# Kernel optimization log

Hardware: AMD Instinct MI355X
Metric: run time of the kernel (lower is better)

Reference implementation:

```python
import jax, jax.numpy as jnp
import numpy as np

B = 4096      # batch
D_IN = 512    # input_dim
D = 256       # d_model
T = 424       # n_targets
L = 6         # num_layers
EPS = 1e-5    # torch LayerNorm default


def _ln(x, g, b):
    m = jnp.mean(x, axis=-1, keepdims=True)
    v = jnp.var(x, axis=-1, keepdims=True)
    return (x - m) * jax.lax.rsqrt(v + EPS) * g + b


def setup_inputs() -> dict:
    key = jax.random.key(0)
    ks = iter(jax.random.split(key, 32))
    r = lambda shape, s=0.05: jax.random.normal(next(ks), shape, dtype=jnp.float32) * s
    return {
        'x': jax.random.normal(next(ks), (B, D_IN), dtype=jnp.float32),
        'proj_W': r((4, D // 4, D_IN)), 'proj_b': r((4, D // 4)),
        'attn_in_W': r((L, 3 * D, D)), 'attn_in_b': r((L, 3 * D)),
        'attn_out_W': r((L, D, D)), 'attn_out_b': r((L, D)),
        'ln_g': jnp.ones((L, D), jnp.float32), 'ln_b': jnp.zeros((L, D), jnp.float32),
        'ff_W1': r((L, 4 * D, D)), 'ff_b1': r((L, 4 * D)),
        'ff_W2': r((L, D, 4 * D)), 'ff_b2': r((L, D)),
        'cross_in_W': r((3 * D, D)), 'cross_in_b': r((3 * D,)),
        'cross_out_W': r((D, D)), 'cross_out_b': r((D,)),
        'tp_W1': r((T, D // 2, D)), 'tp_b1': r((T, D // 2)),
        'tp_ln_g': jnp.ones((T, D // 2), jnp.float32), 'tp_ln_b': jnp.zeros((T, D // 2), jnp.float32),
        'tp_W2': r((T, D // 4, D // 2)), 'tp_b2': r((T, D // 4)),
        'tp_W3': r((T, D // 4)), 'tp_b3': r((T,)),
    }


def reference(x, proj_W, proj_b, attn_in_W, attn_in_b, attn_out_W, attn_out_b,
              ln_g, ln_b, ff_W1, ff_b1, ff_W2, ff_b2,
              cross_in_W, cross_in_b, cross_out_W, cross_out_b,
              tp_W1, tp_b1, tp_ln_g, tp_ln_b, tp_W2, tp_b2, tp_W3, tp_b3):
    # 4 feature projections -> concat == reshape of stacked einsum  [B, 4, D/4] -> [B, D]
    h = jnp.einsum('bd,pkd->bpk', x, proj_W) + proj_b
    h = h.reshape(h.shape[0], D)

    # 6 transformer blocks on seq_len=1: softmax over a single key == 1, so
    # MHA(x,x,x) reduces exactly to out_proj(v_proj(x)); dropout = identity (eval).
    for i in range(L):
        Wv, bv = attn_in_W[i, 2 * D:], attn_in_b[i, 2 * D:]
        attn = (h @ Wv.T + bv) @ attn_out_W[i].T + attn_out_b[i]
        h = _ln(h + attn, ln_g[i], ln_b[i])          # same norm instance reused
        ff = jax.nn.gelu(h @ ff_W1[i].T + ff_b1[i], approximate=False) @ ff_W2[i].T + ff_b2[i]
        h = _ln(h + ff, ln_g[i], ln_b[i])

    # cross-target attention, also seq_len=1 -> v/out projections only
    Wv, bv = cross_in_W[2 * D:], cross_in_b[2 * D:]
    h = h + ((h @ Wv.T + bv) @ cross_out_W.T + cross_out_b)

    # 424 per-target MLP heads, batched as grouped GEMMs
    t = jnp.einsum('bd,tkd->btk', h, tp_W1) + tp_b1          # [B, T, 128]
    t = jax.nn.relu(_ln(t, tp_ln_g, tp_ln_b))
    t = jax.nn.relu(jnp.einsum('btk,tmk->btm', t, tp_W2) + tp_b2)  # [B, T, 64]
    out = jnp.einsum('btm,tm->bt', t, tp_W3) + tp_b3         # [B, T]
    return out
```

## Files before the change

### kernel.cpp

```cpp
#include <hip/hip_runtime.h>
#include <stdint.h>
#include <utility>
#include <type_traits>

using bf16x8 = __attribute__((ext_vector_type(8))) short;
using f32x4  = __attribute__((ext_vector_type(4))) float;

__device__ __forceinline__ f32x4 mfma16(bf16x8 a, bf16x8 b, f32x4 c) {
  return __builtin_amdgcn_mfma_f32_16x16x32_bf16(a, b, c, 0, 0, 0);
}

__device__ __forceinline__ unsigned short f2b_rne(float f) {
  union { float f; unsigned u; } v; v.f = f;
  unsigned r = v.u + 0x7fffu + ((v.u >> 16) & 1u);
  return (unsigned short)(r >> 16);
}

__device__ __forceinline__ void gload16(const void* g, void* l) {
  __builtin_amdgcn_global_load_lds(
      (const __attribute__((address_space(1))) void*)g,
      (__attribute__((address_space(3))) void*)l, 16, 0, 0);
}

template<int N> __device__ __forceinline__ void vmwait() {
  if constexpr (N <= 0)      asm volatile("s_waitcnt vmcnt(0)" ::: "memory");
  else if constexpr (N == 1) asm volatile("s_waitcnt vmcnt(1)" ::: "memory");
  else if constexpr (N == 2) asm volatile("s_waitcnt vmcnt(2)" ::: "memory");
  else if constexpr (N == 3) asm volatile("s_waitcnt vmcnt(3)" ::: "memory");
  else if constexpr (N == 4) asm volatile("s_waitcnt vmcnt(4)" ::: "memory");
  else                       asm volatile("s_waitcnt vmcnt(5)" ::: "memory");
}

template<class F, int... Is>
__device__ __forceinline__ void sfor_impl(F&& f, std::integer_sequence<int, Is...>) {
  (f(std::integral_constant<int, Is>{}), ...);
}
template<int N, class F>
__device__ __forceinline__ void sfor(F&& f) {
  sfor_impl(static_cast<F&&>(f), std::make_integer_sequence<int, N>{});
}

__device__ __forceinline__ void stage1(const unsigned short* __restrict__ W, int K,
                                       int col0, int kt, char* slot, int lane) {
  const int ci = lane >> 2, kc = lane & 3;
  const unsigned short* src = W + (size_t)(col0 + ci) * K + kt * 32
                              + (((kc * 16) ^ ((ci & 3) << 4)) >> 1);
  gload16(src, slot);
}

template<int NCG, int AS, int K>
__device__ __forceinline__ void gemm_pipe3(const unsigned short* __restrict__ W, int c0,
                                           const char* __restrict__ abuf,
                                           char* __restrict__ ring, int lane,
                                           f32x4 (&acc)[NCG]) {
  const int r = lane & 15, hi16 = (lane >> 4) << 4;
  const int swz7 = (r & 7) << 4, swz3 = (r & 3) << 4;
  constexpr int NKT = K / 32;
  constexpr int TILES = NCG * NKT;
  constexpr int DEPTH = (TILES < 5) ? TILES : 5;
  sfor<DEPTH>([&](auto pc) {
    constexpr int p = pc.value;
    stage1(W, K, c0 + (p % NCG) * 16, p / NCG, ring + (p % 6) * 1024, lane);
  });
  bf16x8 areg;
  sfor<TILES>([&](auto tc) {
    constexpr int t = tc.value;
    constexpr int kt = t / NCG, cg = t % NCG;
    constexpr int REM = TILES - 1 - t;
    vmwait<(REM < 4 ? REM : 4)>();
    __builtin_amdgcn_sched_barrier(0);
    if constexpr (t + 5 < TILES) {
      constexpr int t5 = t + 5;
      stage1(W, K, c0 + (t5 % NCG) * 16, t5 / NCG, ring + (t5 % 6) * 1024, lane);
    }
    if constexpr (cg == 0)
      areg = *reinterpret_cast<const bf16x8*>(abuf + r * AS + ((kt * 64 + hi16) ^ swz7));
    const bf16x8 b = *reinterpret_cast<const bf16x8*>(
        ring + (t % 6) * 1024 + r * 64 + (hi16 ^ swz3));
    acc[cg] = mfma16(areg, b, acc[cg]);
  });
}

__global__ void f2b_kernel(const float* __restrict__ s, unsigned short* __restrict__ d, int n4) {
  int i = blockIdx.x * 256 + threadIdx.x;
  if (i >= n4) return;
  float4 v = reinterpret_cast<const float4*>(s)[i];
  ushort4 o;
  o.x = f2b_rne(v.x); o.y = f2b_rne(v.y); o.z = f2b_rne(v.z); o.w = f2b_rne(v.w);
  reinterpret_cast<ushort4*>(d)[i] = o;
}

__global__ __launch_bounds__(256) void compose_attn(
    const float* __restrict__ aiW, const float* __restrict__ aib,
    const float* __restrict__ aoW, const float* __restrict__ aob,
    const float* __restrict__ ciW, const float* __restrict__ cib,
    const float* __restrict__ coW, const float* __restrict__ cob,
    unsigned short* __restrict__ wEff, float* __restrict__ bEff) {
  const int mat = blockIdx.y;
  const float* Wo = (mat < 6) ? aoW + (size_t)mat * 65536 : coW;
  const float* Wv = (mat < 6) ? aiW + (size_t)mat * 196608 + 131072 : ciW + 131072;
  const float* bv = (mat < 6) ? aib + mat * 768 + 512 : cib + 512;
  const float* bo = (mat < 6) ? aob + mat * 256 : cob;
  unsigned short* Wd = wEff + (size_t)mat * 65536;
  const int m = blockIdx.x * 16 + (threadIdx.x >> 4);
  const int k0 = (threadIdx.x & 15) * 16;
  float c[16] = {};
  for (int j = 0; j < 256; ++j) {
    const float a = Wo[m * 256 + j];
    const float* Br = Wv + j * 256 + k0;
#pragma unroll
    for (int kk = 0; kk < 16; ++kk) c[kk] = fmaf(a, Br[kk], c[kk]);
  }
#pragma unroll
  for (int kk = 0; kk < 16; ++kk) Wd[m * 256 + k0 + kk] = f2b_rne(c[kk]);
  if (blockIdx.x == 0) {
    const int mm = threadIdx.x;
    float s = 0.f;
    for (int j = 0; j < 256; ++j) s = fmaf(Wo[mm * 256 + j], bv[j], s);
    bEff[mat * 256 + mm] = s + bo[mm];
  }
}

__global__ __launch_bounds__(1024) void trunk_fused(
    const unsigned short* __restrict__ xb, const unsigned short* __restrict__ pWb,
    const float* __restrict__ projb,
    const unsigned short* __restrict__ wEff, const float* __restrict__ bEff,
    const unsigned short* __restrict__ f1Wb, const float* __restrict__ f1b,
    const unsigned short* __restrict__ f2Wb, const float* __restrict__ f2bp,
    const float* __restrict__ lng, const float* __restrict__ lnb,
    unsigned short* __restrict__ hbf) {
  __shared__ char hbuf[16 * 512];
  __shared__ char gbuf[16 * 2048];
  __shared__ char ringbuf[16 * 6144];
  __shared__ float red[2][16][16];
  const int tid = threadIdx.x, wid = tid >> 6, lane = tid & 63;
  const int r = lane & 15, hi = lane >> 4;
  const int row0 = blockIdx.x << 4;
  const int col = wid * 16 + r;
  char* ring = ringbuf + wid * 6144;

  {
    const int row = tid >> 6, c8 = tid & 63;
    bf16x8 v = *reinterpret_cast<const bf16x8*>(xb + (size_t)(row0 + row) * 512 + c8 * 8);
    *reinterpret_cast<bf16x8*>(gbuf + row * 1024 + ((c8 * 16) ^ ((row & 7) << 4))) = v;
  }
  __syncthreads();

  f32x4 hreg;

  auto store_hb = [&]() {
    const int cb = col * 2;
#pragma unroll
    for (int j = 0; j < 4; ++j) {
      const int row = hi * 4 + j;
      *reinterpret_cast<unsigned short*>(hbuf + row * 512 + (cb ^ ((row & 7) << 4))) =
          f2b_rne(hreg[j]);
    }
  };

  auto ln_apply = [&](float gm, float bb) {
    float sum[4], sq[4];
#pragma unroll
    for (int j = 0; j < 4; ++j) { sum[j] = hreg[j]; sq[j] = hreg[j] * hreg[j]; }
#pragma unroll
    for (int m = 1; m < 16; m <<= 1)
#pragma unroll
      for (int j = 0; j < 4; ++j) {
        sum[j] += __shfl_xor(sum[j], m, 64);
        sq[j]  += __shfl_xor(sq[j],  m, 64);
      }
    if (r == 0)
#pragma unroll
      for (int j = 0; j < 4; ++j) {
        red[0][hi * 4 + j][wid] = sum[j];
        red[1][hi * 4 + j][wid] = sq[j];
      }
    __syncthreads();
#pragma unroll
    for (int j = 0; j < 4; ++j) {
      const int row = hi * 4 + j;
      float ts = 0.f, tq = 0.f;
#pragma unroll
      for (int q = 0; q < 4; ++q) {
        f32x4 p = *reinterpret_cast<const f32x4*>(&red[0][row][q * 4]);
        f32x4 s2 = *reinterpret_cast<const f32x4*>(&red[1][row][q * 4]);
        ts += p[0] + p[1] + p[2] + p[3];
        tq += s2[0] + s2[1] + s2[2] + s2[3];
      }
      const float mean = ts * (1.f / 256.f);
      const float rstd = rsqrtf(tq * (1.f / 256.f) - mean * mean + 1e-5f);
      hreg[j] = (hreg[j] - mean) * rstd * gm + bb;
    }
  };

  {
    f32x4 acc[1] = {};
    gemm_pipe3<1, 1024, 512>(pWb, wid * 16, gbuf, ring, lane, acc);
    const float bv = projb[col];
#pragma unroll
    for (int j = 0; j < 4; ++j) hreg[j] = acc[0][j] + bv;
  }
  store_hb();
  __syncthreads();

  for (int L = 0; L < 6; ++L) {
    const float gm = lng[L * 256 + col], bb = lnb[L * 256 + col];
    {
      f32x4 acc[1] = {};
      gemm_pipe3<1, 512, 256>(wEff + (size_t)L * 65536, wid * 16, hbuf, ring, lane, acc);
      const float be = bEff[L * 256 + col];
#pragma unroll
      for (int j = 0; j < 4; ++j) hreg[j] += acc[0][j] + be;
    }
    ln_apply(gm, bb);
    store_hb();
    __syncthreads();
    {
      f32x4 accf[4] = {};
      gemm_pipe3<4, 512, 256>(f1Wb + (size_t)L * 262144, wid * 64, hbuf, ring, lane, accf);
#pragma unroll
      for (int cf = 0; cf < 4; ++cf) {
        const int colw = wid * 64 + cf * 16 + r;
        const float bv = f1b[L * 1024 + colw];
        const int cb = colw * 2;
#pragma unroll
        for (int j = 0; j < 4; ++j) {
          float y = accf[cf][j] + bv;
          y = 0.5f * y * (1.f + erff(y * 0.70710678118654752f));
          const int row = hi * 4 + j;
          *reinterpret_cast<unsigned short*>(gbuf + row * 2048 + (cb ^ ((row & 7) << 4))) = f2b_rne(y);
        }
      }
    }
    __syncthreads();
    {
      f32x4 acc[1] = {};
      gemm_pipe3<1, 2048, 1024>(f2Wb + (size_t)L * 262144, wid * 16, gbuf, ring, lane, acc);
      const float be = f2bp[L * 256 + col];
#pragma unroll
      for (int j = 0; j < 4; ++j) hreg[j] += acc[0][j] + be;
    }
    ln_apply(gm, bb);
    store_hb();
    __syncthreads();
  }

  {
    f32x4 acc[1] = {};
    gemm_pipe3<1, 512, 256>(wEff + 6ull * 65536, wid * 16, hbuf, ring, lane, acc);
    const float be = bEff[1536 + col];
#pragma unroll
    for (int j = 0; j < 4; ++j) hreg[j] += acc[0][j] + be;
  }
#pragma unroll
  for (int j = 0; j < 4; ++j)
    hbf[(size_t)(row0 + hi * 4 + j) * 256 + col] = f2b_rne(hreg[j]);
}

__global__ __launch_bounds__(512, 2) void phase_d2(
    const unsigned short* __restrict__ hbf, const unsigned short* __restrict__ w1b,
    const float* __restrict__ b1, const float* __restrict__ lng, const float* __restrict__ lnb,
    const unsigned short* __restrict__ w2b, const float* __restrict__ b2,
    const float* __restrict__ w3, const float* __restrict__ b3,
    float* __restrict__ out) {
  __shared__ char sm[149504];
  const int tid = threadIdx.x, wid = tid >> 6, lane = tid & 63;
  const int r = lane & 15, hi = lane >> 4;
  const int sw = (r & 7) << 4;
  const int t = blockIdx.y;

  const unsigned short* w1t = w1b + (size_t)t * 32768;
  const unsigned short* w2t = w2b + (size_t)t * 8192;
#pragma unroll
  for (int i = 0; i < 8; ++i) {
    const int id = tid + i * 512;
    const int c = id >> 5, s = id & 31;
    bf16x8 v = *reinterpret_cast<const bf16x8*>(w1t + c * 256 + s * 8);
    *reinterpret_cast<bf16x8*>(sm + c * 512 + ((s * 16) ^ ((c & 7) << 4))) = v;
  }
#pragma unroll
  for (int i = 0; i < 2; ++i) {
    const int id = tid + i * 512;
    const int c = id >> 4, s = id & 15;
    bf16x8 v = *reinterpret_cast<const bf16x8*>(w2t + c * 128 + s * 8);
    *reinterpret_cast<bf16x8*>(sm + 65536 + c * 256 + ((s * 16) ^ ((c & 7) << 4))) = v;
  }
  {
    float v;
    if (tid < 128)      v = b1 [t * 128 + tid];
    else if (tid < 256) v = lng[t * 128 + tid - 128];
    else if (tid < 384) v = lnb[t * 128 + tid - 256];
    else if (tid < 448) v = b2 [t * 64  + tid - 384];
    else                v = w3 [t * 64  + tid - 448];
    reinterpret_cast<float*>(sm + 81920)[tid] = v;
  }
  __syncthreads();

  const float* cb1 = reinterpret_cast<const float*>(sm + 81920);
  const float* cg  = cb1 + 128;
  const float* cbe = cb1 + 256;
  const float* cb2 = cb1 + 384;
  const float* cw3 = cb1 + 448;
  char* t1w = sm + 83968 + wid * 8192;
  const float b3t = b3[t];
  const int token_b0 = blockIdx.x * 1024;

  for (int tile = 0; tile < 2; ++tile) {
    const int B0 = token_b0 + tile * 512 + wid * 64;

    f32x4 acc1[8][4] = {};
    bf16x8 bc[4], bn[4];
#pragma unroll
    for (int bf = 0; bf < 4; ++bf)
      bc[bf] = *reinterpret_cast<const bf16x8*>(hbf + (size_t)(B0 + bf * 16 + r) * 256 + hi * 8);
#pragma unroll
    for (int ks = 0; ks < 8; ++ks) {
      bf16x8 a[8];
#pragma unroll
      for (int cf = 0; cf < 8; ++cf)
        a[cf] = *reinterpret_cast<const bf16x8*>(sm + (cf * 16 + r) * 512 + ((ks * 64 + hi * 16) ^ sw));
      if (ks < 7) {
#pragma unroll
        for (int bf = 0; bf < 4; ++bf)
          bn[bf] = *reinterpret_cast<const bf16x8*>(hbf + (size_t)(B0 + bf * 16 + r) * 256 + (ks + 1) * 32 + hi * 8);
      }
#pragma unroll
      for (int cf = 0; cf < 8; ++cf)
#pragma unroll
        for (int bf = 0; bf < 4; ++bf)
          acc1[cf][bf] = mfma16(a[cf], bc[bf], acc1[cf][bf]);
#pragma unroll
      for (int bf = 0; bf < 4; ++bf) bc[bf] = bn[bf];
    }

#pragma unroll
    for (int cf = 0; cf < 8; ++cf) {
      f32x4 b1v = *reinterpret_cast<const f32x4*>(cb1 + cf * 16 + hi * 4);
#pragma unroll
      for (int bf = 0; bf < 4; ++bf) acc1[cf][bf] += b1v;
    }

    float mu[4], rsd[4];
#pragma unroll
    for (int bf = 0; bf < 4; ++bf) {
      float s = 0.f, s2 = 0.f;
#pragma unroll
      for (int cf = 0; cf < 8; ++cf)
#pragma unroll
        for (int j = 0; j < 4; ++j) { float v = acc1[cf][bf][j]; s += v; s2 += v * v; }
      s  += __shfl_xor(s, 16, 64);  s  += __shfl_xor(s, 32, 64);
      s2 += __shfl_xor(s2, 16, 64); s2 += __shfl_xor(s2, 32, 64);
      const float m = s * (1.f / 128.f);
      mu[bf] = m;
      rsd[bf] = rsqrtf(s2 * (1.f / 128.f) - m * m + 1e-5f);
    }

    f32x4 acc2[4][4] = {};
#pragma unroll
    for (int half = 0; half < 2; ++half) {
#pragma unroll
      for (int cf = 0; cf < 8; ++cf) {
        f32x4 gv = *reinterpret_cast<const f32x4*>(cg  + cf * 16 + hi * 4);
        f32x4 bv = *reinterpret_cast<const f32x4*>(cbe + cf * 16 + hi * 4);
#pragma unroll
        for (int bl = 0; bl < 2; ++bl) {
          const int bf = half * 2 + bl;
          unsigned o01, o23;
          {
            float y0 = fmaxf((acc1[cf][bf][0] - mu[bf]) * rsd[bf] * gv[0] + bv[0], 0.f);
            float y1 = fmaxf((acc1[cf][bf][1] - mu[bf]) * rsd[bf] * gv[1] + bv[1], 0.f);
            float y2 = fmaxf((acc1[cf][bf][2] - mu[bf]) * rsd[bf] * gv[2] + bv[2], 0.f);
            float y3 = fmaxf((acc1[cf][bf][3] - mu[bf]) * rsd[bf] * gv[3] + bv[3], 0.f);
            o01 = (unsigned)f2b_rne(y0) | ((unsigned)f2b_rne(y1) << 16);
            o23 = (unsigned)f2b_rne(y2) | ((unsigned)f2b_rne(y3) << 16);
          }
          uint2 pk; pk.x = o01; pk.y = o23;
          *reinterpret_cast<uint2*>(t1w + (bl * 16 + r) * 256 + ((cf * 32 + hi * 8) ^ sw)) = pk;
        }
      }
#pragma unroll
      for (int ks = 0; ks < 4; ++ks) {
        bf16x8 a2[4];
#pragma unroll
        for (int cf2 = 0; cf2 < 4; ++cf2)
          a2[cf2] = *reinterpret_cast<const bf16x8*>(sm + 65536 + (cf2 * 16 + r) * 256 + ((ks * 64 + hi * 16) ^ sw));
#pragma unroll
        for (int bl = 0; bl < 2; ++bl) {
          bf16x8 bb = *reinterpret_cast<const bf16x8*>(t1w + (bl * 16 + r) * 256 + ((ks * 64 + hi * 16) ^ sw));
#pragma unroll
          for (int cf2 = 0; cf2 < 4; ++cf2)
            acc2[cf2][half * 2 + bl] = mfma16(a2[cf2], bb, acc2[cf2][half * 2 + bl]);
        }
      }
    }

    float s[4] = {0.f, 0.f, 0.f, 0.f};
#pragma unroll
    for (int cf2 = 0; cf2 < 4; ++cf2) {
      f32x4 b2v = *reinterpret_cast<const f32x4*>(cb2 + cf2 * 16 + hi * 4);
      f32x4 w3v = *reinterpret_cast<const f32x4*>(cw3 + cf2 * 16 + hi * 4);
#pragma unroll
      for (int bf = 0; bf < 4; ++bf)
#pragma unroll
        for (int j = 0; j < 4; ++j)
          s[bf] += fmaxf(acc2[cf2][bf][j] + b2v[j], 0.f) * w3v[j];
    }
#pragma unroll
    for (int bf = 0; bf < 4; ++bf) {
      s[bf] += __shfl_xor(s[bf], 16, 64);
      s[bf] += __shfl_xor(s[bf], 32, 64);
      if (hi == 0) out[(size_t)(B0 + bf * 16 + r) * 424 + t] = s[bf] + b3t;
    }
  }
}

extern "C" void kernel_launch(void* const* d_in, const int* in_sizes, int n_in,
                              void* d_out, int out_size, void* d_ws, size_t ws_size,
                              hipStream_t stream) {
  const float* x     = (const float*)d_in[0];
  const float* projW = (const float*)d_in[1];
  const float* projb = (const float*)d_in[2];
  const float* aiW   = (const float*)d_in[3];
  const float* aib   = (const float*)d_in[4];
  const float* aoW   = (const float*)d_in[5];
  const float* aob   = (const float*)d_in[6];
  const float* lng   = (const float*)d_in[7];
  const float* lnbp  = (const float*)d_in[8];
  const float* f1W   = (const float*)d_in[9];
  const float* f1b   = (const float*)d_in[10];
  const float* f2W   = (const float*)d_in[11];
  const float* f2bp  = (const float*)d_in[12];
  const float* ciW   = (const float*)d_in[13];
  const float* cib   = (const float*)d_in[14];
  const float* coW   = (const float*)d_in[15];
  const float* cob   = (const float*)d_in[16];
  const float* tpW1  = (const float*)d_in[17];
  const float* tpb1  = (const float*)d_in[18];
  const float* tplng = (const float*)d_in[19];
  const float* tplnb = (const float*)d_in[20];
  const float* tpW2  = (const float*)d_in[21];
  const float* tpb2  = (const float*)d_in[22];
  const float* tpW3  = (const float*)d_in[23];
  const float* tpb3  = (const float*)d_in[24];
  float* out = (float*)d_out;

  char* ws = (char*)d_ws;
  size_t off = 0;
  auto alloc = [&](size_t n) { char* p = ws + off; off = (off + n + 255) & ~(size_t)255; return p; };
  unsigned short* xb   = (unsigned short*)alloc(4096ull * 512 * 2);
  unsigned short* pWb  = (unsigned short*)alloc(256ull * 512 * 2);
  unsigned short* f1Wb = (unsigned short*)alloc(6ull * 1024 * 256 * 2);
  unsigned short* f2Wb = (unsigned short*)alloc(6ull * 256 * 1024 * 2);
  unsigned short* W1b  = (unsigned short*)alloc(424ull * 128 * 256 * 2);
  unsigned short* W2b  = (unsigned short*)alloc(424ull * 64 * 128 * 2);
  unsigned short* wEff = (unsigned short*)alloc(7ull * 256 * 256 * 2);
  float*          bEff = (float*)alloc(7ull * 256 * 4);
  unsigned short* hbf  = (unsigned short*)alloc(4096ull * 256 * 2);

  auto conv = [&](const float* s, unsigned short* d, size_t n) {
    int n4 = (int)(n >> 2);
    f2b_kernel<<<dim3((n4 + 255) / 256), dim3(256), 0, stream>>>(s, d, n4);
  };
  compose_attn<<<dim3(16, 7), dim3(256), 0, stream>>>(aiW, aib, aoW, aob, ciW, cib, coW, cob, wEff, bEff);
  conv(x, xb, 4096ull * 512);
  conv(projW, pWb, 256ull * 512);
  conv(f1W, f1Wb, 6ull * 1024 * 256);
  conv(f2W, f2Wb, 6ull * 256 * 1024);
  conv(tpW1, W1b, 424ull * 128 * 256);
  conv(tpW2, W2b, 424ull * 64 * 128);

  trunk_fused<<<dim3(256), dim3(1024), 0, stream>>>(
      xb, pWb, projb, wEff, bEff, f1Wb, f1b, f2Wb, f2bp, lng, lnbp, hbf);

  phase_d2<<<dim3(4, 424), dim3(512), 0, stream>>>(hbf, W1b, tpb1, tplng, tplnb, W2b, tpb2, tpW3, tpb3, out);
}
```

Baseline: 537.0 us.

## Stream trunk GEMM weights directly into registers instead of LDS ring

Replaces the per-wave LDS ring, filled by global_load_lds, with direct global-to-register loads of weight fragments, using a prefetch depth of 7 held in a small register array. This drops 96KB of shared memory and the LDS read per MFMA, which could raise occupancy and cut LDS traffic. In exchange it uses more VGPRs, and the global loads are 16-byte per-lane row reads that may coalesce less well.

New measurement: 611.0 us. 1.14x slower.

```diff
diff --git a/kernel.cpp b/kernel.cpp
--- a/kernel.cpp
+++ b/kernel.cpp
@@ -16,19 +16,16 @@
   return (unsigned short)(r >> 16);
 }
 
-__device__ __forceinline__ void gload16(const void* g, void* l) {
-  __builtin_amdgcn_global_load_lds(
-      (const __attribute__((address_space(1))) void*)g,
-      (__attribute__((address_space(3))) void*)l, 16, 0, 0);
-}
-
 template<int N> __device__ __forceinline__ void vmwait() {
-  if constexpr (N <= 0)      asm volatile("s_waitcnt vmcnt(0)" ::: "memory");
+  static_assert(N >= 0 && N <= 7, "");
+  if constexpr (N == 0)      asm volatile("s_waitcnt vmcnt(0)" ::: "memory");
   else if constexpr (N == 1) asm volatile("s_waitcnt vmcnt(1)" ::: "memory");
   else if constexpr (N == 2) asm volatile("s_waitcnt vmcnt(2)" ::: "memory");
   else if constexpr (N == 3) asm volatile("s_waitcnt vmcnt(3)" ::: "memory");
   else if constexpr (N == 4) asm volatile("s_waitcnt vmcnt(4)" ::: "memory");
-  else                       asm volatile("s_waitcnt vmcnt(5)" ::: "memory");
+  else if constexpr (N == 5) asm volatile("s_waitcnt vmcnt(5)" ::: "memory");
+  else if constexpr (N == 6) asm volatile("s_waitcnt vmcnt(6)" ::: "memory");
+  else                       asm volatile("s_waitcnt vmcnt(7)" ::: "memory");
 }
 
 template<class F, int... Is>
@@ -40,44 +37,43 @@
   sfor_impl(static_cast<F&&>(f), std::make_integer_sequence<int, N>{});
 }
 
-__device__ __forceinline__ void stage1(const unsigned short* __restrict__ W, int K,
-                                       int col0, int kt, char* slot, int lane) {
-  const int ci = lane >> 2, kc = lane & 3;
-  const unsigned short* src = W + (size_t)(col0 + ci) * K + kt * 32
-                              + (((kc * 16) ^ ((ci & 3) << 4)) >> 1);
-  gload16(src, slot);
-}
-
 template<int NCG, int AS, int K>
-__device__ __forceinline__ void gemm_pipe3(const unsigned short* __restrict__ W, int c0,
-                                           const char* __restrict__ abuf,
-                                           char* __restrict__ ring, int lane,
-                                           f32x4 (&acc)[NCG]) {
-  const int r = lane & 15, hi16 = (lane >> 4) << 4;
-  const int swz7 = (r & 7) << 4, swz3 = (r & 3) << 4;
+__device__ __forceinline__ void gemm_regs(const unsigned short* __restrict__ W, int c0,
+                                          const char* __restrict__ abuf, int lane,
+                                          f32x4 (&acc)[NCG]) {
+  const int r = lane & 15, hi = lane >> 4;
+  const int hi16 = hi << 4;
+  const int swz7 = (r & 7) << 4;
   constexpr int NKT = K / 32;
   constexpr int TILES = NCG * NKT;
-  constexpr int DEPTH = (TILES < 5) ? TILES : 5;
-  sfor<DEPTH>([&](auto pc) {
+  constexpr int D = (TILES < 7) ? TILES : 7;
+  const unsigned short* base[NCG];
+#pragma unroll
+  for (int cg = 0; cg < NCG; ++cg)
+    base[cg] = W + (size_t)(c0 + cg * 16 + r) * K + hi * 8;
+
+  bf16x8 w[8];
+  sfor<D>([&](auto pc) {
     constexpr int p = pc.value;
-    stage1(W, K, c0 + (p % NCG) * 16, p / NCG, ring + (p % 6) * 1024, lane);
+    w[p % 8] = *reinterpret_cast<const bf16x8*>(base[p % NCG] + (p / NCG) * 32);
+    __builtin_amdgcn_sched_barrier(0);
   });
+
   bf16x8 areg;
   sfor<TILES>([&](auto tc) {
     constexpr int t = tc.value;
     constexpr int kt = t / NCG, cg = t % NCG;
     constexpr int REM = TILES - 1 - t;
-    vmwait<(REM < 4 ? REM : 4)>();
+    vmwait<(REM < D - 1 ? REM : D - 1)>();
     __builtin_amdgcn_sched_barrier(0);
-    if constexpr (t + 5 < TILES) {
-      constexpr int t5 = t + 5;
-      stage1(W, K, c0 + (t5 % NCG) * 16, t5 / NCG, ring + (t5 % 6) * 1024, lane);
-    }
     if constexpr (cg == 0)
       areg = *reinterpret_cast<const bf16x8*>(abuf + r * AS + ((kt * 64 + hi16) ^ swz7));
-    const bf16x8 b = *reinterpret_cast<const bf16x8*>(
-        ring + (t % 6) * 1024 + r * 64 + (hi16 ^ swz3));
-    acc[cg] = mfma16(areg, b, acc[cg]);
+    acc[cg] = mfma16(areg, w[t % 8], acc[cg]);
+    if constexpr (t + D < TILES) {
+      constexpr int tD = t + D;
+      w[tD % 8] = *reinterpret_cast<const bf16x8*>(base[tD % NCG] + (tD / NCG) * 32);
+      __builtin_amdgcn_sched_barrier(0);
+    }
   });
 }
 
@@ -131,13 +127,11 @@
     unsigned short* __restrict__ hbf) {
   __shared__ char hbuf[16 * 512];
   __shared__ char gbuf[16 * 2048];
-  __shared__ char ringbuf[16 * 6144];
   __shared__ float red[2][16][16];
   const int tid = threadIdx.x, wid = tid >> 6, lane = tid & 63;
   const int r = lane & 15, hi = lane >> 4;
   const int row0 = blockIdx.x << 4;
   const int col = wid * 16 + r;
-  char* ring = ringbuf + wid * 6144;
 
   {
     const int row = tid >> 6, c8 = tid & 63;
@@ -195,7 +189,7 @@
 
   {
     f32x4 acc[1] = {};
-    gemm_pipe3<1, 1024, 512>(pWb, wid * 16, gbuf, ring, lane, acc);
+    gemm_regs<1, 1024, 512>(pWb, wid * 16, gbuf, lane, acc);
     const float bv = projb[col];
 #pragma unroll
     for (int j = 0; j < 4; ++j) hreg[j] = acc[0][j] + bv;
@@ -207,7 +201,7 @@
     const float gm = lng[L * 256 + col], bb = lnb[L * 256 + col];
     {
       f32x4 acc[1] = {};
-      gemm_pipe3<1, 512, 256>(wEff + (size_t)L * 65536, wid * 16, hbuf, ring, lane, acc);
+      gemm_regs<1, 512, 256>(wEff + (size_t)L * 65536, wid * 16, hbuf, lane, acc);
       const float be = bEff[L * 256 + col];
 #pragma unroll
       for (int j = 0; j < 4; ++j) hreg[j] += acc[0][j] + be;
@@ -217,7 +211,7 @@
     __syncthreads();
     {
       f32x4 accf[4] = {};
-      gemm_pipe3<4, 512, 256>(f1Wb + (size_t)L * 262144, wid * 64, hbuf, ring, lane, accf);
+      gemm_regs<4, 512, 256>(f1Wb + (size_t)L * 262144, wid * 64, hbuf, lane, accf);
 #pragma unroll
       for (int cf = 0; cf < 4; ++cf) {
         const int colw = wid * 64 + cf * 16 + r;
@@ -235,7 +229,7 @@
     __syncthreads();
     {
       f32x4 acc[1] = {};
-      gemm_pipe3<1, 2048, 1024>(f2Wb + (size_t)L * 262144, wid * 16, gbuf, ring, lane, acc);
+      gemm_regs<1, 2048, 1024>(f2Wb + (size_t)L * 262144, wid * 16, gbuf, lane, acc);
       const float be = f2bp[L * 256 + col];
 #pragma unroll
       for (int j = 0; j < 4; ++j) hreg[j] += acc[0][j] + be;
@@ -247,7 +241,7 @@
 
   {
     f32x4 acc[1] = {};
-    gemm_pipe3<1, 512, 256>(wEff + 6ull * 65536, wid * 16, hbuf, ring, lane, acc);
+    gemm_regs<1, 512, 256>(wEff + 6ull * 65536, wid * 16, hbuf, lane, acc);
     const float be = bEff[1536 + col];
 #pragma unroll
     for (int j = 0; j < 4; ++j) hreg[j] += acc[0][j] + be;
```
